# Optimization experiments

Hardware: AMD Instinct MI355X
Metric: run time of the kernel (lower is better)

## Reference

```python
import jax, jax.numpy as jnp
import numpy as np

SIZE = 256

def _linear(x, W, b):
    # torch nn.Linear: y = x @ W^T + b, W has shape [out, in]
    return jnp.einsum('bsd,ed->bse', x, W) + b

def setup_inputs() -> dict:
    key = jax.random.key(0)
    ks = jax.random.split(key, 10)
    B, Sq, Sk, D = 8, 2048, 2048, SIZE
    s = 1.0 / np.sqrt(D)
    return {
        'x': jax.random.normal(ks[0], (B, Sq, D), jnp.float32),
        'states': jax.random.normal(ks[1], (B, Sk, D), jnp.float32),
        'Wq': jax.random.normal(ks[2], (D, D), jnp.float32) * s,
        'bq': jnp.zeros((D,), jnp.float32),
        'Wk': jax.random.normal(ks[3], (D, D), jnp.float32) * s,
        'bk': jnp.zeros((D,), jnp.float32),
        'Wv': jax.random.normal(ks[4], (D, D), jnp.float32) * s,
        'bv': jnp.zeros((D,), jnp.float32),
        'Wa': jax.random.normal(ks[5], (D, D), jnp.float32) * s,  # LuongAttention.fc
        'ba': jnp.zeros((D,), jnp.float32),
    }

def reference(x, states, Wq, bq, Wk, bk, Wv, bv, Wa, ba):
    q = _linear(x, Wq, bq)          # [B,Sq,D]
    k = _linear(states, Wk, bk)     # [B,Sk,D]
    v = _linear(states, Wv, bv)     # [B,Sk,D]
    wk = _linear(k, Wa, ba)         # [B,Sk,D]
    scores = jnp.einsum('bqd,bkd->bqk', q, wk)   # bmm(q, wk^T)
    scores = jax.nn.softmax(scores, axis=-1)
    # original: (v[:,None,:,:] * scores[...,None]).sum(-2) == matmul
    context = jnp.einsum('bqk,bkd->bqd', scores, v)
    return context
```

## Files before the change

### kernel.cpp

```cpp
#include <hip/hip_runtime.h>
#include <cstdint>
#include <cstddef>

typedef _Float16 half_t;
typedef _Float16 half8 __attribute__((ext_vector_type(8)));
typedef _Float16 half4v __attribute__((ext_vector_type(4)));
typedef float float4_ __attribute__((ext_vector_type(4)));

#define NB 8
#define SEQ 2048
#define DIM 256
#define NROWS (NB*SEQ)
#define KS 4
#define NIT 16

__device__ __forceinline__ void dma16(const half_t* g, half_t* l) {
    __builtin_amdgcn_global_load_lds(
        (const __attribute__((address_space(1))) void*)g,
        (__attribute__((address_space(3))) void*)l,
        16, 0, 0);
}

__global__ __launch_bounds__(256) void prep_kernel(
    const float* __restrict__ Wq, const float* __restrict__ Wk,
    const float* __restrict__ Wv, const float* __restrict__ Wa,
    const float* __restrict__ bq,
    half_t* __restrict__ M_hi, half_t* __restrict__ M_lo,
    half_t* __restrict__ Wk_hi, half_t* __restrict__ Wk_lo,
    half_t* __restrict__ Wv_hi, float* __restrict__ bq2)
{
    const int d = blockIdx.x;
    const int m = threadIdx.x;
    const int idx = d * 256 + m;
    float acc = 0.f;
    for (int e = 0; e < 256; ++e)
        acc += Wa[e * 256 + d] * Wq[e * 256 + m];
    half_t h = (half_t)acc;
    M_hi[idx] = h;
    M_lo[idx] = (half_t)(acc - (float)h);
    float wk = Wk[idx];
    h = (half_t)wk;
    Wk_hi[idx] = h;
    Wk_lo[idx] = (half_t)(wk - (float)h);
    Wv_hi[idx] = (half_t)Wv[idx];
    if (m == 0) {
        float b2 = 0.f;
        for (int e = 0; e < 256; ++e) b2 += bq[e] * Wa[e * 256 + d];
        bq2[d] = b2;
    }
}

__global__ __launch_bounds__(256, 2) void linear_kernel(
    const float* __restrict__ x, const float* __restrict__ states,
    const half_t* __restrict__ M_hi, const half_t* __restrict__ M_lo, const float* __restrict__ bq2,
    const half_t* __restrict__ Wk_hi, const half_t* __restrict__ Wk_lo, const float* __restrict__ bk,
    const half_t* __restrict__ Wv_hi, const float* __restrict__ bv,
    half_t* __restrict__ q2_hi,
    half_t* __restrict__ k_hi,
    half_t* __restrict__ vT)
{
    __shared__ half_t sB[2 * 64 * 256];
    half_t* sBh = sB;
    half_t* sBl = sB + 64 * 256;

    const int seg  = blockIdx.x >> 8;
    const int t    = blockIdx.x & 255;
    const int tid  = threadIdx.x;
    const int lane = tid & 63;
    const int wv   = tid >> 6;
    const int quad = lane >> 4;
    const int l15  = lane & 15;
    const int rb   = t * 64;
    const int r0   = rb + wv * 16;

    const float* src  = (seg == 0) ? x : states;
    const half_t* Bh  = (seg == 0) ? M_hi : (seg == 1) ? Wk_hi : Wv_hi;
    const half_t* Bl  = (seg == 0) ? M_lo : Wk_lo;
    const float* bias = (seg == 0) ? bq2 : (seg == 1) ? bk : bv;

    half8 ah[8], al[8];
    #pragma unroll
    for (int c = 0; c < 8; ++c) {
        const float* pa = src + (size_t)(r0 + l15) * 256 + c * 32 + quad * 8;
        float4_ u0 = *(const float4_*)pa;
        float4_ u1 = *(const float4_*)(pa + 4);
        #pragma unroll
        for (int j = 0; j < 4; ++j) {
            half_t hh = (half_t)u0[j];
            ah[c][j] = hh; al[c][j] = (half_t)(u0[j] - (float)hh);
            hh = (half_t)u1[j];
            ah[c][4 + j] = hh; al[c][4 + j] = (half_t)(u1[j] - (float)hh);
        }
    }

    float4_ acc[16];
    if (seg != 2) {
        #pragma unroll
        for (int nt = 0; nt < 16; ++nt) {
            float be = bias[nt * 16 + l15];
            acc[nt] = {be, be, be, be};
        }
    } else {
        #pragma unroll
        for (int et = 0; et < 16; ++et)
            #pragma unroll
            for (int r = 0; r < 4; ++r)
                acc[et][r] = bias[et * 16 + quad * 4 + r];
    }

    #pragma unroll
    for (int eg = 0; eg < 4; ++eg) {
        __syncthreads();
        #pragma unroll
        for (int i = 0; i < 8; ++i) {
            int g = tid + i * 256;
            int e = g >> 5, c = g & 31;
            *(half8*)(sBh + e * 256 + ((c ^ (e & 7)) * 8)) =
                *(const half8*)(Bh + (size_t)(eg * 64 + e) * 256 + c * 8);
        }
        if (seg != 2) {
            #pragma unroll
            for (int i = 0; i < 8; ++i) {
                int g = tid + i * 256;
                int e = g >> 5, c = g & 31;
                *(half8*)(sBl + e * 256 + ((c ^ (e & 7)) * 8)) =
                    *(const half8*)(Bl + (size_t)(eg * 64 + e) * 256 + c * 8);
            }
        }
        __syncthreads();

        if (seg != 2) {
            #pragma unroll
            for (int ntl = 0; ntl < 4; ++ntl) {
                float4_ a = acc[eg * 4 + ntl];
                const int el = ntl * 16 + l15;
                #pragma unroll
                for (int c = 0; c < 8; ++c) {
                    int off = el * 256 + (((c * 4 + quad) ^ (el & 7)) * 8);
                    half8 bh = *(const half8*)(sBh + off);
                    half8 bl = *(const half8*)(sBl + off);
                    a = __builtin_amdgcn_mfma_f32_16x16x32_f16(ah[c], bh, a, 0, 0, 0);
                    a = __builtin_amdgcn_mfma_f32_16x16x32_f16(al[c], bh, a, 0, 0, 0);
                    a = __builtin_amdgcn_mfma_f32_16x16x32_f16(ah[c], bl, a, 0, 0, 0);
                }
                acc[eg * 4 + ntl] = a;
            }
        } else {
            #pragma unroll
            for (int ntl = 0; ntl < 4; ++ntl) {
                float4_ a = acc[eg * 4 + ntl];
                const int el = ntl * 16 + l15;
                #pragma unroll
                for (int c = 0; c < 8; ++c) {
                    int off = el * 256 + (((c * 4 + quad) ^ (el & 7)) * 8);
                    half8 aw = *(const half8*)(sBh + off);
                    a = __builtin_amdgcn_mfma_f32_16x16x32_f16(aw, ah[c], a, 0, 0, 0);
                }
                acc[eg * 4 + ntl] = a;
            }
        }
    }

    __syncthreads();
    if (seg != 2) {
        half_t* R = sB;
        #pragma unroll
        for (int nt = 0; nt < 16; ++nt)
            #pragma unroll
            for (int r = 0; r < 4; ++r)
                R[(wv * 16 + quad * 4 + r) * 256 + nt * 16 + l15] = (half_t)acc[nt][r];
        __syncthreads();
        if (seg == 0) {
            for (int i = 0; i < 8; ++i) {
                int g = tid + i * 256;
                int row = g >> 5, cc = g & 31;
                *(half8*)(q2_hi + (size_t)(rb + row) * 256 + cc * 8) =
                    *(const half8*)(R + row * 256 + cc * 8);
            }
        } else {
            for (int i = 0; i < 8; ++i) {
                int g = tid + i * 256;
                int row = g >> 5, cc = g & 31;
                int s = row & 31;
                size_t dst = ((size_t)(rb + row) >> 5) * 8192 + s * 256 + ((cc ^ (s & 7)) * 8);
                *(half8*)(k_hi + dst) = *(const half8*)(R + row * 256 + cc * 8);
            }
        }
    } else {
        half_t* sV = sB;
        #pragma unroll
        for (int et = 0; et < 16; ++et)
            #pragma unroll
            for (int r = 0; r < 4; ++r)
                sV[(et * 16 + quad * 4 + r) * 68 + wv * 16 + l15] = (half_t)acc[et][r];
        __syncthreads();
        const int b = rb >> 11, s0 = rb & 2047;
        for (int i = 0; i < 8; ++i) {
            int g = tid + i * 256;
            int d = g >> 3, sc8 = g & 7;
            int kt = (s0 >> 5) + (sc8 >> 2);
            int q  = sc8 & 3;
            int t32 = (sc8 >> 2) * 32;
            int slot = q ^ (d & 3) ^ ((d >> 2) & 3);
            half4v a4 = *(const half4v*)(sV + d * 68 + t32 + q * 4);
            half4v b4 = *(const half4v*)(sV + d * 68 + t32 + 16 + q * 4);
            half8 hv;
            hv[0] = a4[0]; hv[1] = a4[1]; hv[2] = a4[2]; hv[3] = a4[3];
            hv[4] = b4[0]; hv[5] = b4[1]; hv[6] = b4[2]; hv[7] = b4[3];
            size_t dst = ((size_t)b * 64 + kt) * 8192 + d * 32 + slot * 8;
            *(half8*)(vT + dst) = hv;
        }
    }
}

__global__ __launch_bounds__(256, 2) void attn_kernel(
    const half_t* __restrict__ q2_hi,
    const half_t* __restrict__ k_hi, const half_t* __restrict__ vT,
    half_t* __restrict__ pc, float* __restrict__ pm, float* __restrict__ pl)
{
    __shared__ __align__(16) unsigned char smem[64 * 1024];
    float* scr = (float*)smem;

    const int tid  = threadIdx.x;
    const int lane = tid & 63;
    const int wv   = tid >> 6;
    const int quad = lane >> 4;
    const int l15  = lane & 15;

    const int b  = blockIdx.x & 7;
    const int qt = (blockIdx.x >> 3) & 15;
    const int ks = blockIdx.x >> 7;

    const int qbase = b * 2048 + qt * 128 + wv * 32;

    half8 qf[2][8];
    #pragma unroll
    for (int ct = 0; ct < 2; ++ct)
        #pragma unroll
        for (int c = 0; c < 8; ++c)
            qf[ct][c] = *(const half8*)(q2_hi +
                (size_t)(qbase + ct * 16 + l15) * 256 + c * 32 + quad * 8);

    float4_ ctx[16][2];
    #pragma unroll
    for (int dt = 0; dt < 16; ++dt) {
        ctx[dt][0] = {0.f, 0.f, 0.f, 0.f};
        ctx[dt][1] = {0.f, 0.f, 0.f, 0.f};
    }
    float m_c[2] = {-1e30f, -1e30f};
    float l_c[2] = {0.f, 0.f};

    const half_t* kh_b = k_hi + (size_t)b * 64 * 8192;
    const half_t* vt_b = vT   + (size_t)b * 64 * 8192;
    const int t0 = ks * NIT;

    const int vslot8 = (quad ^ (l15 & 3) ^ ((l15 >> 2) & 3)) * 8;

    {
        const half_t* kt_ = kh_b + (size_t)t0 * 8192;
        const half_t* vt_ = vt_b + (size_t)t0 * 8192;
        #pragma unroll
        for (int i = 0; i < 4; ++i) {
            const int sg = i * 4 + wv;
            dma16(kt_ + sg * 512 + lane * 8, (half_t*)smem + sg * 512);
            dma16(vt_ + sg * 512 + lane * 8, (half_t*)(smem + 32768) + sg * 512);
        }
    }

    for (int it = 0; it < NIT; ++it) {
        half_t* s_k  = (half_t*)(smem + ((it & 1) << 14));
        half_t* s_v  = (half_t*)(smem + 32768 + ((it & 1) << 14));
        half_t* s_kn = (half_t*)(smem + (((it + 1) & 1) << 14));
        half_t* s_vn = (half_t*)(smem + 32768 + (((it + 1) & 1) << 14));
        const bool pre = (it + 1 < NIT);

        asm volatile("s_waitcnt vmcnt(0)" ::: "memory");
        __builtin_amdgcn_s_barrier();
        asm volatile("" ::: "memory");

        if (pre) {
            const half_t* kt_ = kh_b + (size_t)(t0 + it + 1) * 8192;
            const half_t* vt_ = vt_b + (size_t)(t0 + it + 1) * 8192;
            #pragma unroll
            for (int i = 0; i < 4; ++i) {
                const int sg = i * 4 + wv;
                dma16(kt_ + sg * 512 + lane * 8, s_kn + sg * 512);
                dma16(vt_ + sg * 512 + lane * 8, s_vn + sg * 512);
            }
        }

        float4_ S[2][2];
        S[0][0] = {0.f,0.f,0.f,0.f}; S[0][1] = {0.f,0.f,0.f,0.f};
        S[1][0] = {0.f,0.f,0.f,0.f}; S[1][1] = {0.f,0.f,0.f,0.f};
        __builtin_amdgcn_s_setprio(1);
        #pragma unroll
        for (int c = 0; c < 8; ++c)
            #pragma unroll
            for (int kt = 0; kt < 2; ++kt) {
                const int key = kt * 16 + l15;
                const int off = key * 256 + (((c * 4 + quad) ^ (key & 7)) * 8);
                half8 kf = *(const half8*)(s_k + off);
                #pragma unroll
                for (int ct = 0; ct < 2; ++ct)
                    S[kt][ct] = __builtin_amdgcn_mfma_f32_16x16x32_f16(kf, qf[ct][c], S[kt][ct], 0, 0, 0);
            }
        __builtin_amdgcn_s_setprio(0);
        __builtin_amdgcn_sched_barrier(0);

        float mx0, mx1;
        {
            float a0 = fmaxf(fmaxf(S[0][0][0], S[0][0][1]), fmaxf(S[0][0][2], S[0][0][3]));
            float b0 = fmaxf(fmaxf(S[1][0][0], S[1][0][1]), fmaxf(S[1][0][2], S[1][0][3]));
            mx0 = fmaxf(a0, b0);
            mx0 = fmaxf(mx0, __shfl_xor(mx0, 16));
            mx0 = fmaxf(mx0, __shfl_xor(mx0, 32));
            float a1 = fmaxf(fmaxf(S[0][1][0], S[0][1][1]), fmaxf(S[0][1][2], S[0][1][3]));
            float b1 = fmaxf(fmaxf(S[1][1][0], S[1][1][1]), fmaxf(S[1][1][2], S[1][1][3]));
            mx1 = fmaxf(a1, b1);
            mx1 = fmaxf(mx1, __shfl_xor(mx1, 16));
            mx1 = fmaxf(mx1, __shfl_xor(mx1, 32));
        }
        const int doresc = __any((mx0 > m_c[0] + 8.f) || (mx1 > m_c[1] + 8.f));
        float alpha0 = 1.f, alpha1 = 1.f;
        if (doresc) {
            float mn0 = fmaxf(m_c[0], mx0);
            float mn1 = fmaxf(m_c[1], mx1);
            alpha0 = __expf(m_c[0] - mn0);
            alpha1 = __expf(m_c[1] - mn1);
            m_c[0] = mn0; m_c[1] = mn1;
        }
        half8 pf[2];
        #pragma unroll
        for (int ct = 0; ct < 2; ++ct) {
            const float mm = m_c[ct];
            float rs = 0.f;
            #pragma unroll
            for (int r = 0; r < 4; ++r) {
                float p0 = __expf(S[0][ct][r] - mm);
                float p1 = __expf(S[1][ct][r] - mm);
                rs += p0 + p1;
                pf[ct][r]     = (half_t)p0;
                pf[ct][4 + r] = (half_t)p1;
            }
            rs += __shfl_xor(rs, 16);
            rs += __shfl_xor(rs, 32);
            l_c[ct] = l_c[ct] * (ct ? alpha1 : alpha0) + rs;
        }
        if (doresc) {
            #pragma unroll
            for (int dt = 0; dt < 16; ++dt)
                #pragma unroll
                for (int r = 0; r < 4; ++r) {
                    ctx[dt][0][r] *= alpha0;
                    ctx[dt][1][r] *= alpha1;
                }
        }

        __builtin_amdgcn_s_setprio(1);
        #pragma unroll
        for (int dt = 0; dt < 16; ++dt) {
            half8 vf = *(const half8*)(s_v + (dt * 16 + l15) * 32 + vslot8);
            ctx[dt][0] = __builtin_amdgcn_mfma_f32_16x16x32_f16(vf, pf[0], ctx[dt][0], 0, 0, 0);
            ctx[dt][1] = __builtin_amdgcn_mfma_f32_16x16x32_f16(vf, pf[1], ctx[dt][1], 0, 0, 0);
        }
        __builtin_amdgcn_s_setprio(0);
        __builtin_amdgcn_sched_barrier(0);
    }

    __syncthreads();

    float rinv[2] = {1.0f / l_c[0], 1.0f / l_c[1]};
    float* sw = scr + wv * (32 * 68);
    half_t* pcs = pc + (size_t)ks * NROWS * 256;
    #pragma unroll
    for (int rd = 0; rd < 4; ++rd) {
        #pragma unroll
        for (int dtl = 0; dtl < 4; ++dtl) {
            const int dt = rd * 4 + dtl;
            #pragma unroll
            for (int ct = 0; ct < 2; ++ct)
                #pragma unroll
                for (int r = 0; r < 4; ++r)
                    sw[(ct * 16 + l15) * 68 + dtl * 16 + quad * 4 + r] = ctx[dt][ct][r] * rinv[ct];
        }
        #pragma unroll
        for (int i = 0; i < 8; ++i) {
            int g = lane + i * 64;
            int q = g >> 4, dc = g & 15;
            float4_ v4 = *(const float4_*)(sw + q * 68 + dc * 4);
            half4v h4;
            #pragma unroll
            for (int j = 0; j < 4; ++j) h4[j] = (half_t)v4[j];
            *(half4v*)(pcs + (size_t)(qbase + q) * 256 + rd * 64 + dc * 4) = h4;
        }
    }
    if (quad == 0) {
        #pragma unroll
        for (int ct = 0; ct < 2; ++ct) {
            const size_t row = qbase + ct * 16 + l15;
            pm[(size_t)ks * NROWS + row] = m_c[ct];
            pl[(size_t)ks * NROWS + row] = l_c[ct];
        }
    }
}

__global__ __launch_bounds__(256) void combine_kernel(
    const half_t* __restrict__ pc, const float* __restrict__ pm,
    const float* __restrict__ pl, float* __restrict__ out)
{
    const int t = threadIdx.x;
    const int row = blockIdx.x * 4 + (t >> 6);
    const int d0 = (t & 63) * 4;
    float m[KS], l[KS];
    float ms = -1e30f;
    #pragma unroll
    for (int i = 0; i < KS; ++i) {
        m[i] = pm[(size_t)i * NROWS + row];
        l[i] = pl[(size_t)i * NROWS + row];
        ms = fmaxf(ms, m[i]);
    }
    float w[KS], tot = 0.f;
    #pragma unroll
    for (int i = 0; i < KS; ++i) {
        w[i] = l[i] * __expf(m[i] - ms);
        tot += w[i];
    }
    float inv = 1.0f / tot;
    float4_ o = {0.f, 0.f, 0.f, 0.f};
    #pragma unroll
    for (int i = 0; i < KS; ++i) {
        half4v y = *(const half4v*)(pc + ((size_t)i * NROWS + row) * 256 + d0);
        float wi = w[i] * inv;
        #pragma unroll
        for (int j = 0; j < 4; ++j) o[j] += wi * (float)y[j];
    }
    *(float4_*)(out + (size_t)row * 256 + d0) = o;
}

extern "C" void kernel_launch(void* const* d_in, const int* in_sizes, int n_in,
                              void* d_out, int out_size, void* d_ws, size_t ws_size,
                              hipStream_t stream) {
    const float* x      = (const float*)d_in[0];
    const float* states = (const float*)d_in[1];
    const float* Wq     = (const float*)d_in[2];
    const float* bq     = (const float*)d_in[3];
    const float* Wk     = (const float*)d_in[4];
    const float* bk     = (const float*)d_in[5];
    const float* Wv     = (const float*)d_in[6];
    const float* bv     = (const float*)d_in[7];
    const float* Wa     = (const float*)d_in[8];
    float* out = (float*)d_out;

    char* ws = (char*)d_ws;
    size_t off = 0;
    auto alloc = [&](size_t bytes) -> void* {
        void* p = ws + off;
        off += (bytes + 255) & ~(size_t)255;
        return p;
    };
    half_t* M_hi  = (half_t*)alloc(65536 * 2);
    half_t* M_lo  = (half_t*)alloc(65536 * 2);
    half_t* Wk_hi = (half_t*)alloc(65536 * 2);
    half_t* Wk_lo = (half_t*)alloc(65536 * 2);
    half_t* Wv_hi = (half_t*)alloc(65536 * 2);
    float*  bq2   = (float*)alloc(256 * 4);
    half_t* q2_hi = (half_t*)alloc((size_t)NROWS * 256 * 2);
    half_t* k_hi  = (half_t*)alloc((size_t)NROWS * 256 * 2);
    half_t* vT    = (half_t*)alloc((size_t)NROWS * 256 * 2);
    half_t* pc    = (half_t*)alloc((size_t)KS * NROWS * 256 * 2);
    float*  pm    = (float*)alloc((size_t)KS * NROWS * 4);
    float*  pl    = (float*)alloc((size_t)KS * NROWS * 4);

    prep_kernel<<<256, 256, 0, stream>>>(Wq, Wk, Wv, Wa, bq,
                                         M_hi, M_lo, Wk_hi, Wk_lo, Wv_hi, bq2);
    linear_kernel<<<768, 256, 0, stream>>>(x, states,
                                           M_hi, M_lo, bq2,
                                           Wk_hi, Wk_lo, bk,
                                           Wv_hi, bv,
                                           q2_hi, k_hi, vT);
    attn_kernel<<<8 * 16 * KS, 256, 0, stream>>>(q2_hi, k_hi, vT,
                                                 pc, pm, pl);
    combine_kernel<<<NROWS / 4, 256, 0, stream>>>(pc, pm, pl, out);
}
```

Baseline: 198.1 us.

## Software-pipeline P·V MFMA of previous tile with current softmax and split K/V prefetch

The P·V matrix multiply for tile it-1 is deferred into iteration it, where it runs between the QK^T MFMAs and the exponentials of the current tile, so matrix and transcendental work can interleave. K and V prefetches are now issued separately. The wait at the top of the loop uses vmcnt(4), so it only blocks on the K tile, and the V prefetch moves after a second barrier at the end of the iteration. A final P·V epilogue runs after the loop, and the trailing __syncthreads is replaced by an earlier barrier. This adds an extra barrier per iteration, keeps previous P fragments live in registers, and risks reusing scratch memory while other waves still read V.

```diff
diff --git a/kernel.cpp b/kernel.cpp
--- a/kernel.cpp
+++ b/kernel.cpp
@@ -258,34 +258,41 @@
 
     {
         const half_t* kt_ = kh_b + (size_t)t0 * 8192;
-        const half_t* vt_ = vt_b + (size_t)t0 * 8192;
         #pragma unroll
         for (int i = 0; i < 4; ++i) {
             const int sg = i * 4 + wv;
             dma16(kt_ + sg * 512 + lane * 8, (half_t*)smem + sg * 512);
+        }
+        const half_t* vt_ = vt_b + (size_t)t0 * 8192;
+        #pragma unroll
+        for (int i = 0; i < 4; ++i) {
+            const int sg = i * 4 + wv;
             dma16(vt_ + sg * 512 + lane * 8, (half_t*)(smem + 32768) + sg * 512);
         }
     }
+
+    half8 pfp[2];
+    #pragma unroll
+    for (int ct = 0; ct < 2; ++ct)
+        #pragma unroll
+        for (int j = 0; j < 8; ++j) pfp[ct][j] = (half_t)0;
 
     for (int it = 0; it < NIT; ++it) {
         half_t* s_k  = (half_t*)(smem + ((it & 1) << 14));
-        half_t* s_v  = (half_t*)(smem + 32768 + ((it & 1) << 14));
-        half_t* s_kn = (half_t*)(smem + (((it + 1) & 1) << 14));
-        half_t* s_vn = (half_t*)(smem + 32768 + (((it + 1) & 1) << 14));
+        half_t* s_vP = (half_t*)(smem + 32768 + (((it + 1) & 1) << 14));
         const bool pre = (it + 1 < NIT);
 
-        asm volatile("s_waitcnt vmcnt(0)" ::: "memory");
+        asm volatile("s_waitcnt vmcnt(4)" ::: "memory");
         __builtin_amdgcn_s_barrier();
         asm volatile("" ::: "memory");
 
         if (pre) {
             const half_t* kt_ = kh_b + (size_t)(t0 + it + 1) * 8192;
-            const half_t* vt_ = vt_b + (size_t)(t0 + it + 1) * 8192;
+            half_t* kdst = (half_t*)(smem + (((it + 1) & 1) << 14));
             #pragma unroll
             for (int i = 0; i < 4; ++i) {
                 const int sg = i * 4 + wv;
-                dma16(kt_ + sg * 512 + lane * 8, s_kn + sg * 512);
-                dma16(vt_ + sg * 512 + lane * 8, s_vn + sg * 512);
+                dma16(kt_ + sg * 512 + lane * 8, kdst + sg * 512);
             }
         }
 
@@ -305,7 +312,6 @@
                     S[kt][ct] = __builtin_amdgcn_mfma_f32_16x16x32_f16(kf, qf[ct][c], S[kt][ct], 0, 0, 0);
             }
         __builtin_amdgcn_s_setprio(0);
-        __builtin_amdgcn_sched_barrier(0);
 
         float mx0, mx1;
         {
@@ -329,7 +335,18 @@
             alpha1 = __expf(m_c[1] - mn1);
             m_c[0] = mn0; m_c[1] = mn1;
         }
-        half8 pf[2];
+
+        __builtin_amdgcn_s_setprio(1);
+        if (it > 0) {
+            #pragma unroll
+            for (int dt = 0; dt < 16; ++dt) {
+                half8 vf = *(const half8*)(s_vP + (dt * 16 + l15) * 32 + vslot8);
+                ctx[dt][0] = __builtin_amdgcn_mfma_f32_16x16x32_f16(vf, pfp[0], ctx[dt][0], 0, 0, 0);
+                ctx[dt][1] = __builtin_amdgcn_mfma_f32_16x16x32_f16(vf, pfp[1], ctx[dt][1], 0, 0, 0);
+            }
+        }
+
+        half8 pfc[2];
         #pragma unroll
         for (int ct = 0; ct < 2; ++ct) {
             const float mm = m_c[ct];
@@ -339,13 +356,15 @@
                 float p0 = __expf(S[0][ct][r] - mm);
                 float p1 = __expf(S[1][ct][r] - mm);
                 rs += p0 + p1;
-                pf[ct][r]     = (half_t)p0;
-                pf[ct][4 + r] = (half_t)p1;
+                pfc[ct][r]     = (half_t)p0;
+                pfc[ct][4 + r] = (half_t)p1;
             }
             rs += __shfl_xor(rs, 16);
             rs += __shfl_xor(rs, 32);
             l_c[ct] = l_c[ct] * (ct ? alpha1 : alpha0) + rs;
         }
+        __builtin_amdgcn_s_setprio(0);
+
         if (doresc) {
             #pragma unroll
             for (int dt = 0; dt < 16; ++dt)
@@ -356,18 +375,37 @@
                 }
         }
 
+        pfp[0] = pfc[0];
+        pfp[1] = pfc[1];
+
+        if (pre) {
+            __builtin_amdgcn_sched_barrier(0);
+            __builtin_amdgcn_s_barrier();
+            asm volatile("" ::: "memory");
+            const half_t* vt_ = vt_b + (size_t)(t0 + it + 1) * 8192;
+            half_t* vdst = (half_t*)(smem + 32768 + (((it + 1) & 1) << 14));
+            #pragma unroll
+            for (int i = 0; i < 4; ++i) {
+                const int sg = i * 4 + wv;
+                dma16(vt_ + sg * 512 + lane * 8, vdst + sg * 512);
+            }
+        }
+    }
+
+    asm volatile("s_waitcnt vmcnt(0)" ::: "memory");
+    __builtin_amdgcn_s_barrier();
+    asm volatile("" ::: "memory");
+    {
+        half_t* s_v = (half_t*)(smem + 32768 + (((NIT - 1) & 1) << 14));
         __builtin_amdgcn_s_setprio(1);
         #pragma unroll
         for (int dt = 0; dt < 16; ++dt) {
             half8 vf = *(const half8*)(s_v + (dt * 16 + l15) * 32 + vslot8);
-            ctx[dt][0] = __builtin_amdgcn_mfma_f32_16x16x32_f16(vf, pf[0], ctx[dt][0], 0, 0, 0);
-            ctx[dt][1] = __builtin_amdgcn_mfma_f32_16x16x32_f16(vf, pf[1], ctx[dt][1], 0, 0, 0);
+            ctx[dt][0] = __builtin_amdgcn_mfma_f32_16x16x32_f16(vf, pfp[0], ctx[dt][0], 0, 0, 0);
+            ctx[dt][1] = __builtin_amdgcn_mfma_f32_16x16x32_f16(vf, pfp[1], ctx[dt][1], 0, 0, 0);
         }
         __builtin_amdgcn_s_setprio(0);
-        __builtin_amdgcn_sched_barrier(0);
-    }
-
-    __syncthreads();
+    }
 
     float rinv[2] = {1.0f / l_c[0], 1.0f / l_c[1]};
     float* sw = scr + wv * (32 * 68);
```

After: 196.8 us. No clear change (-0.7%).
